# Optimization experiments

Hardware: AMD Instinct MI355X
Metric: run time of the kernel (lower is better)

## Reference

```python
import jax, jax.numpy as jnp
import numpy as np

NHEAD = 8  # heads (module default)


def _ln(x, g, b):
    m = x.mean(-1, keepdims=True)
    v = ((x - m) ** 2).mean(-1, keepdims=True)
    return (x - m) / jnp.sqrt(v + 1e-5) * g + b


def setup_inputs() -> dict:
    B, N, D, L, JE = 256, 133, 256, 6, 32
    DIN = 2 + 3 + JE  # in_proj input dim
    ks = jax.random.split(jax.random.key(0), 16)
    # chain skeleton adjacency (connected) + Floyd-Warshall hop distances
    a = np.zeros((N, N), np.float32)
    i = np.arange(N - 1)
    a[i, i + 1] = 1.0
    a[i + 1, i] = 1.0
    dist = np.full((N, N), 1e6, np.float32)
    dist[a > 0] = 1.0
    np.fill_diagonal(dist, 0.0)
    for kk in range(N):
        dist = np.minimum(dist, dist[:, kk:kk + 1] + dist[kk:kk + 1, :])
    w = lambda k, sh: jax.random.normal(k, sh, jnp.float32) * 0.02
    return dict(
        x2d=jax.random.normal(ks[0], (B, N, 2), jnp.float32),
        y3d=jax.random.normal(ks[1], (B, N, 3), jnp.float32),
        joint_emb=w(ks[2], (N, JE)),
        in_w=w(ks[3], (DIN, D)), in_b=jnp.zeros((D,), jnp.float32),
        cls_tok=w(ks[4], (1, 1, D)),
        noedge_bias=jnp.float32(-2.0), deg_scale=jnp.float32(0.2), gamma=jnp.float32(0.8),
        v2n=jnp.zeros((1,), jnp.float32), n2v=jnp.zeros((1,), jnp.float32), vself=jnp.zeros((1,), jnp.float32),
        ln1_g=jnp.ones((L, D), jnp.float32), ln1_b=jnp.zeros((L, D), jnp.float32),
        wq=w(ks[5], (L, D, D)), bq=jnp.zeros((L, D), jnp.float32),
        wk=w(ks[6], (L, D, D)), bk=jnp.zeros((L, D), jnp.float32),
        wv=w(ks[7], (L, D, D)), bv=jnp.zeros((L, D), jnp.float32),
        wo=w(ks[8], (L, D, D)), bo=jnp.zeros((L, D), jnp.float32),
        ln2_g=jnp.ones((L, D), jnp.float32), ln2_b=jnp.zeros((L, D), jnp.float32),
        mlp_w1=w(ks[9], (L, D, D)), mlp_b1=jnp.zeros((L, D), jnp.float32),  # mlp_ratio=1.0 -> hidden=D
        mlp_w2=w(ks[10], (L, D, D)), mlp_b2=jnp.zeros((L, D), jnp.float32),
        lnf_g=jnp.ones((D,), jnp.float32), lnf_b=jnp.zeros((D,), jnp.float32),
        head_w1=w(ks[11], (D, D)), head_b1=jnp.zeros((D,), jnp.float32),
        head_w2=w(ks[12], (D, 1)), head_b2=jnp.zeros((1,), jnp.float32),
        adj=jnp.asarray(a), dist=jnp.asarray(dist),
    )


def reference(x2d, y3d, joint_emb, in_w, in_b, cls_tok, noedge_bias, deg_scale, gamma,
              v2n, n2v, vself, ln1_g, ln1_b, wq, bq, wk, bk, wv, bv, wo, bo,
              ln2_g, ln2_b, mlp_w1, mlp_b1, mlp_w2, mlp_b2, lnf_g, lnf_b,
              head_w1, head_b1, head_w2, head_b2, adj, dist):
    B, N, _ = x2d.shape
    D = in_w.shape[1]
    dk = D // NHEAD
    T = N + 1
    # token features: [x2d, y3d, joint_embedding(arange(N))]
    je = jnp.broadcast_to(joint_emb[None], (B, N, joint_emb.shape[-1]))
    z = jnp.concatenate([x2d, y3d, je], axis=-1) @ in_w + in_b            # (B,N,D)
    z = jnp.concatenate([jnp.broadcast_to(cls_tok, (B, 1, D)), z], axis=1)  # (B,T,D)
    # graph attention bias (soft mask + degree + SPD + VNode 'replace'); (T,T), broadcast over B,H
    deg = adj.sum(-1)
    e = -gamma * dist                                                      # SPD term (gamma learnable)
    e = jnp.where(adj > 0, e, e + noedge_bias)                             # soft non-edge penalty
    e = e + deg_scale * (deg[:, None] + deg[None, :]) / (deg.max() + 1e-6)
    bias = jnp.zeros((T, T), jnp.float32)
    bias = bias.at[1:, 1:].set(e)
    bias = bias.at[0, 1:].set(v2n[0])
    bias = bias.at[1:, 0].set(n2v[0])
    bias = bias.at[0, 0].set(vself[0])
    bias = bias[None, None]                                                # (1,1,T,T)
    inv_sqrt_dk = jnp.float32(1.0 / np.sqrt(dk))

    def block(zc, p):
        g1, b1, qw, qb, kw, kb, vw, vb, ow, ob, g2, b2, w1, bb1, w2, bb2 = p
        x = _ln(zc, g1, b1)
        q = (x @ qw + qb).reshape(B, T, NHEAD, dk)
        k = (x @ kw + kb).reshape(B, T, NHEAD, dk)
        v = (x @ vw + vb).reshape(B, T, NHEAD, dk)
        scores = jnp.einsum('bthd,bshd->bhts', q, k) * inv_sqrt_dk + bias  # (B,H,T,T)
        attn = jax.nn.softmax(scores, axis=-1)
        out = jnp.einsum('bhts,bshd->bthd', attn, v).reshape(B, T, D)
        zc = zc + out @ ow + ob
        x = _ln(zc, g2, b2)
        zc = zc + jax.nn.gelu(x @ w1 + bb1, approximate=False) @ w2 + bb2
        return zc, None

    z, _ = jax.lax.scan(block, z, (ln1_g, ln1_b, wq, bq, wk, bk, wv, bv, wo, bo,
                                   ln2_g, ln2_b, mlp_w1, mlp_b1, mlp_w2, mlp_b2))
    z = _ln(z, lnf_g, lnf_b)
    c = z[:, 0]                                                            # CLS token
    h = jax.nn.gelu(c @ head_w1 + head_b1, approximate=False)
    return h @ head_w2 + head_b2                                           # (B,1) energy
```

## Files before the change

kernel.cpp:

```cpp
#include <hip/hip_runtime.h>
#include <stdint.h>

typedef unsigned short u16;
typedef unsigned int   u32;
typedef short bf16x8 __attribute__((ext_vector_type(8)));
typedef float f32x4  __attribute__((ext_vector_type(4)));

#define NLAYER 6
#define T_TOK  134
#define MROWS  34304
#define QKV_E  196608
#define O_E    65536
#define LSTR_E 393216
#define HEAD_E_OFF 2359296
#define SPV 168

__device__ __forceinline__ float b2f(u16 u){ u32 x=((u32)u)<<16; return __builtin_bit_cast(float,x); }
__device__ __forceinline__ u16 f2b(float f){ u32 x=__builtin_bit_cast(u32,f); return (u16)((x + 0x7fffu + ((x>>16)&1u))>>16); }
__device__ __forceinline__ void mfma16(f32x4& c, bf16x8 a, bf16x8 b){
  asm("v_mfma_f32_16x16x32_bf16 %0, %1, %2, %0" : "+v"(c) : "v"(a), "v"(b));
}
__device__ __forceinline__ float gelu_f(float x){ return 0.5f*x*(1.0f+erff(x*0.70710678118654752f)); }
__device__ __forceinline__ void gload16(const u16* g, u16* l){
  __builtin_amdgcn_global_load_lds((const __attribute__((address_space(1))) u32*)g,
                                   (__attribute__((address_space(3))) u32*)l, 16, 0, 0);
}

__global__ __launch_bounds__(256) void prep_k(
    const float* __restrict__ wq, const float* __restrict__ wk, const float* __restrict__ wv,
    const float* __restrict__ wo, const float* __restrict__ w1, const float* __restrict__ w2,
    const float* __restrict__ hw1,
    const float* __restrict__ bq, const float* __restrict__ bk, const float* __restrict__ bv,
    u16* __restrict__ wpack, float* __restrict__ bqkv)
{
  const int cid = blockIdx.x*256 + threadIdx.x;
  if (cid < 294912 + 8192) {
    const float* msrc = nullptr; int NT, c, layer = 0, isqkv = 0;
    if (cid >= 294912){ msrc = hw1; NT = 16; c = cid - 294912; }
    else {
      layer = cid / 49152; int r = cid - layer*49152;
      if      (r < 24576){ NT = 48; c = r;          isqkv = 1; }
      else if (r < 32768){ NT = 16; c = r - 24576;  msrc = wo + layer*65536; }
      else if (r < 40960){ NT = 16; c = r - 32768;  msrc = w1 + layer*65536; }
      else               { NT = 16; c = r - 40960;  msrc = w2 + layer*65536; }
    }
    const int lane = c & 63, ctkk = c >> 6;
    const int ct = ctkk % NT, kk = ctkk / NT;
    const int k = kk*32 + (lane>>4)*8;
    const int n = ct*16 + (lane&15);
    u16 ov[8];
    if (isqkv){
      const int sub = n >> 8, nn = n & 255;
      const float* s3 = (sub==0 ? wq : (sub==1 ? wk : wv)) + layer*65536;
#pragma unroll
      for(int j=0;j<8;j++) ov[j] = f2b(s3[(size_t)(k+j)*256 + nn]);
    } else {
#pragma unroll
      for(int j=0;j<8;j++) ov[j] = f2b(msrc[(size_t)(k+j)*256 + n]);
    }
    *(uint4*)(wpack + (size_t)cid*8) = *(uint4*)ov;
  } else {
    const int id = cid - 303104;
    if (id >= 0 && id < 576){
#pragma unroll
      for(int j=0;j<8;j++){
        const int p = id*8 + j; const int layer = p/768; const int w = p - layer*768;
        bqkv[p] = (w<256) ? bq[layer*256+w] : (w<512) ? bk[layer*256+w-256] : bv[layer*256+w-512];
      }
    }
  }
}

__global__ __launch_bounds__(256) void deg_k(const float* __restrict__ adj, float* __restrict__ degb)
{
  __shared__ float deg[133];
  const int tid = threadIdx.x;
  if (tid < 133){
    float s = 0.f;
    for (int j=0;j<133;j++) s += adj[tid*133+j];
    deg[tid] = s; degb[tid] = s;
  }
  __syncthreads();
  if (tid == 0){ float m=0.f; for (int i=0;i<133;i++) m = fmaxf(m, deg[i]); degb[133] = 1.0f/(m + 1e-6f); }
}

__global__ __launch_bounds__(256) void bias_k(
    const float* __restrict__ adj, const float* __restrict__ dist, const float* __restrict__ degb,
    const float* __restrict__ gamma, const float* __restrict__ noedge,
    const float* __restrict__ dscale, const float* __restrict__ v2n,
    const float* __restrict__ n2v, const float* __restrict__ vself,
    float* __restrict__ biasP)
{
  const int idx = blockIdx.x*256 + threadIdx.x;
  if (idx >= 144*144) return;
  const int t = idx/144, s = idx - t*144;
  float v;
  if (s >= 134)          v = -1e30f;
  else if (t >= 134)     v = 0.f;
  else if (t==0 && s==0) v = vself[0];
  else if (t==0)         v = v2n[0];
  else if (s==0)         v = n2v[0];
  else {
    const int i = t-1, j = s-1;
    float e = -gamma[0]*dist[i*133+j];
    if (!(adj[i*133+j] > 0.f)) e += noedge[0];
    e += dscale[0]*(degb[i]+degb[j])*degb[133];
    v = e;
  }
  biasP[idx] = v;
}

__global__ __launch_bounds__(256) void embed_k(
    const float* __restrict__ x2d, const float* __restrict__ y3d,
    const float* __restrict__ je,  const float* __restrict__ inw,
    const float* __restrict__ inb, const float* __restrict__ cls,
    float* __restrict__ z)
{
  __shared__ float f[4][37];
  const int tid = threadIdx.x, g = tid>>6, lane = tid & 63;
  const int r = blockIdx.x*4 + g;
  const int b = r/134, t = r - b*134;
  if (t > 0 && lane < 37){
    const int n = t - 1;
    float v;
    if (lane < 2)      v = x2d[(size_t)(b*133+n)*2 + lane];
    else if (lane < 5) v = y3d[(size_t)(b*133+n)*3 + (lane-2)];
    else               v = je[(size_t)n*32 + (lane-5)];
    f[g][lane] = v;
  }
  __syncthreads();
  const int d4 = lane*4;
  float4 o;
  if (t == 0){
    o = *(const float4*)(cls + d4);
  } else {
    o = *(const float4*)(inb + d4);
#pragma unroll
    for (int i=0;i<37;i++){
      const float fv = f[g][i];
      const float4 w = *(const float4*)(inw + i*256 + d4);
      o.x += fv*w.x; o.y += fv*w.y; o.z += fv*w.z; o.w += fv*w.w;
    }
  }
  *(float4*)(z + (size_t)r*256 + d4) = o;
}

__global__ __launch_bounds__(256) void ln_k(
    const float* __restrict__ z, const float* __restrict__ gw, const float* __restrict__ bw,
    u16* __restrict__ out, int rmul)
{
  const int row = blockIdx.x*8 + (threadIdx.x>>5);
  const int t5 = threadIdx.x & 31;
  const float* zr = z + (size_t)row*rmul*256 + t5*8;
  float4 v0 = *(const float4*)zr;
  float4 v1 = *(const float4*)(zr+4);
  float s = v0.x+v0.y+v0.z+v0.w + v1.x+v1.y+v1.z+v1.w;
#pragma unroll
  for (int m=1;m<32;m<<=1) s += __shfl_xor(s, m, 32);
  const float mean = s*(1.f/256.f);
  float d0=v0.x-mean,d1=v0.y-mean,d2=v0.z-mean,d3=v0.w-mean;
  float d4=v1.x-mean,d5=v1.y-mean,d6=v1.z-mean,d7=v1.w-mean;
  float q = d0*d0+d1*d1+d2*d2+d3*d3+d4*d4+d5*d5+d6*d6+d7*d7;
#pragma unroll
  for (int m=1;m<32;m<<=1) q += __shfl_xor(q, m, 32);
  const float rstd = rsqrtf(q*(1.f/256.f) + 1e-5f);
  const int c = t5*8;
  float4 g0 = *(const float4*)(gw+c), g1 = *(const float4*)(gw+c+4);
  float4 b0 = *(const float4*)(bw+c), b1 = *(const float4*)(bw+c+4);
  u32 p0 = (u32)f2b(d0*rstd*g0.x+b0.x) | ((u32)f2b(d1*rstd*g0.y+b0.y)<<16);
  u32 p1 = (u32)f2b(d2*rstd*g0.z+b0.z) | ((u32)f2b(d3*rstd*g0.w+b0.w)<<16);
  u32 p2 = (u32)f2b(d4*rstd*g1.x+b1.x) | ((u32)f2b(d5*rstd*g1.y+b1.y)<<16);
  u32 p3 = (u32)f2b(d6*rstd*g1.z+b1.z) | ((u32)f2b(d7*rstd*g1.w+b1.w)<<16);
  uint4 ov; ov.x=p0; ov.y=p1; ov.z=p2; ov.w=p3;
  *(uint4*)(out + (size_t)row*256 + c) = ov;
}

template<int EPI>
__global__ __launch_bounds__(256) void gemm_k(
    const u16* __restrict__ A, const u16* __restrict__ PB, const float* __restrict__ bias,
    u16* __restrict__ Obf, float* __restrict__ Of, float* __restrict__ Z, int NT)
{
  const int N = NT*16;
  __shared__ __align__(16) u16 lsA[4096];
  __shared__ __align__(16) u16 lsB[4096];
  const int tid = threadIdx.x, lane = tid & 63, wid = tid >> 6;
  const int m0 = blockIdx.x*128, n0 = blockIdx.y*128;
  const int wr = wid >> 1, wc = wid & 1;
  f32x4 acc[4][4];
#pragma unroll
  for (int i=0;i<4;i++)
#pragma unroll
    for (int j=0;j<4;j++){ acc[i][j][0]=0.f; acc[i][j][1]=0.f; acc[i][j][2]=0.f; acc[i][j][3]=0.f; }

  const u16* gA0 = A + (size_t)(m0 + wid*32 + (lane&15))*256 + (lane>>4)*8;
  const u16* gA1 = gA0 + 16*256;
  u16* lA0 = lsA + wid*1024;
  u16* lA1 = lA0 + 512;
  const size_t bstr = (size_t)NT*512;
  const u16* gB0 = PB + ((size_t)((n0>>4) + wid)*64 + lane)*8;
  const u16* gB1 = gB0 + 4*512;
  u16* lB0 = lsB + wid*512;
  u16* lB1 = lB0 + 4*512;

  for (int kk=0; kk<8; ++kk){
    gload16(gA0 + kk*32, lA0);
    gload16(gA1 + kk*32, lA1);
    gload16(gB0 + (size_t)kk*bstr, lB0);
    gload16(gB1 + (size_t)kk*bstr, lB1);
    __syncthreads();
    bf16x8 af[4], bfr[4];
#pragma unroll
    for (int mi=0;mi<4;mi++) af[mi]  = *(const bf16x8*)(lsA + ((wr*4+mi)*64 + lane)*8);
#pragma unroll
    for (int ni=0;ni<4;ni++) bfr[ni] = *(const bf16x8*)(lsB + ((wc*4+ni)*64 + lane)*8);
#pragma unroll
    for (int mi=0;mi<4;mi++)
#pragma unroll
      for (int ni=0;ni<4;ni++)
        mfma16(acc[mi][ni], af[mi], bfr[ni]);
    __syncthreads();
  }
  const int r0 = (lane>>4)*4, c15 = lane & 15;
#pragma unroll
  for (int mi=0;mi<4;mi++){
#pragma unroll
    for (int ni=0;ni<4;ni++){
      const int col = n0 + wc*64 + ni*16 + c15;
      const float bv = bias[col];
#pragma unroll
      for (int r=0;r<4;r++){
        const int row = m0 + wr*64 + mi*16 + r0 + r;
        float v = acc[mi][ni][r] + bv;
        if constexpr (EPI==0){ Obf[(size_t)row*N + col] = f2b(v); }
        else if constexpr (EPI==1){ Z[(size_t)row*256 + col] += v; }
        else if constexpr (EPI==2){ Obf[(size_t)row*N + col] = f2b(gelu_f(v)); }
        else { Of[(size_t)row*N + col] = gelu_f(v); }
      }
    }
  }
}

__global__ __launch_bounds__(192, 3) void attn_k(
    const u16* __restrict__ qkv, const float* __restrict__ biasP, u16* __restrict__ ao)
{
  const int blk = blockIdx.x, b = blk >> 3, h = blk & 7;
  __shared__ __align__(16) u16 Pf[3*2560];
  __shared__ __align__(16) u16 Vt[32*SPV];
  const int tid = threadIdx.x, lane = tid & 63, w = tid >> 6;
  const int g = lane >> 4, c15 = lane & 15;
  const size_t base = (size_t)b*134*768 + h*32;

  if (tid < 134){
    const uint4* vr = (const uint4*)(qkv + base + (size_t)tid*768 + 512);
    uint4 w0=vr[0], w1=vr[1], w2=vr[2], w3=vr[3];
    u32 wa[8] = {w0.x,w0.y,w0.z,w0.w,w1.x,w1.y,w1.z,w1.w};
    u32 wb[8] = {w2.x,w2.y,w2.z,w2.w,w3.x,w3.y,w3.z,w3.w};
#pragma unroll
    for (int k=0;k<8;k++){
      Vt[(2*k  )*SPV + tid] = (u16)(wa[k] & 0xffffu);
      Vt[(2*k+1)*SPV + tid] = (u16)(wa[k] >> 16);
      Vt[(16+2*k  )*SPV + tid] = (u16)(wb[k] & 0xffffu);
      Vt[(16+2*k+1)*SPV + tid] = (u16)(wb[k] >> 16);
    }
  } else if (tid < 160){
#pragma unroll
    for (int d=0; d<32; d++) Vt[d*SPV + tid] = 0;
  }
  u16* Pfw = Pf + w*2560;
  const int c_r = 2*(c15>>2) + (g&1) + 8*(2*(c15&3) + (g>>1));
  if (lane >= 32){ uint4 zz; zz.x=0u; zz.y=0u; zz.z=0u; zz.w=0u;
                   *(uint4*)(Pfw + 4*512 + c_r*8) = zz; }
  __syncthreads();

  bf16x8 kf[9];
  const int kg = g*8;
#pragma unroll
  for (int st=0; st<9; st++){
    int sr = st*16 + c15; if (sr > 133) sr = 133;
    kf[st] = *(const bf16x8*)(qkv + base + (size_t)sr*768 + 256 + kg);
  }
  const float isq = 0.17677669529663687f;

  for (int i=0;i<3;i++){
    const int qt = 3*w + i;
    int qr = qt*16 + c15; if (qr > 133) qr = 133;
    const bf16x8 qf = *(const bf16x8*)(qkv + base + (size_t)qr*768 + kg);
    f32x4 s_[9];
#pragma unroll
    for (int st=0; st<9; st++){
      s_[st][0]=0.f; s_[st][1]=0.f; s_[st][2]=0.f; s_[st][3]=0.f;
      mfma16(s_[st], qf, kf[st]);
    }
    asm volatile("s_waitcnt lgkmcnt(0)" ::: "memory");
    const int hi = c15 >> 3, j7 = c15 & 7;
#pragma unroll
    for (int r=0;r<4;r++){
      const float* br = biasP + (size_t)(qt*16 + g*4 + r)*144 + c15;
      float v[9];
#pragma unroll
      for (int st=0; st<9; st++) v[st] = s_[st][r]*isq + br[st*16];
      float mx = v[0];
#pragma unroll
      for (int st=1; st<9; st++) mx = fmaxf(mx, v[st]);
      mx = fmaxf(mx, __shfl_xor(mx,1)); mx = fmaxf(mx, __shfl_xor(mx,2));
      mx = fmaxf(mx, __shfl_xor(mx,4)); mx = fmaxf(mx, __shfl_xor(mx,8));
      float sum = 0.f;
#pragma unroll
      for (int st=0; st<9; st++){ v[st] = __expf(v[st]-mx); sum += v[st]; }
      sum += __shfl_xor(sum,1); sum += __shfl_xor(sum,2);
      sum += __shfl_xor(sum,4); sum += __shfl_xor(sum,8);
      const float ivs = 1.0f/sum;
#pragma unroll
      for (int st=0; st<9; st++){
        const int hi2 = (2*st + hi) & 3;
        const int cw  = 2*g + (hi2 & 1) + 8*(2*r + (hi2 >> 1));
        Pfw[(st>>1)*512 + cw*8 + j7] = f2b(v[st]*ivs);
      }
    }
    asm volatile("s_waitcnt lgkmcnt(0)" ::: "memory");
    __builtin_amdgcn_sched_barrier(0);
    bf16x8 a5[5];
#pragma unroll
    for (int ks=0; ks<5; ks++) a5[ks] = *(const bf16x8*)(Pfw + ks*512 + c_r*8);
#pragma unroll
    for (int nt=0; nt<2; nt++){
      f32x4 o; o[0]=0.f; o[1]=0.f; o[2]=0.f; o[3]=0.f;
#pragma unroll
      for (int ks=0; ks<5; ks++){
        const bf16x8 vb = *(const bf16x8*)(Vt + (nt*16 + c15)*SPV + ks*32 + kg);
        mfma16(o, a5[ks], vb);
      }
#pragma unroll
      for (int r=0;r<4;r++){
        const int q = qt*16 + g*4 + r;
        if (q < 134) ao[((size_t)(b*134+q))*256 + h*32 + nt*16 + c15] = f2b(o[r]);
      }
    }
  }
}

__global__ __launch_bounds__(256) void head_out_k(
    const float* __restrict__ h, const float* __restrict__ w2,
    const float* __restrict__ b2, float* __restrict__ out)
{
  const int b = blockIdx.x, d = threadIdx.x;
  float v = h[(size_t)b*256 + d] * w2[d];
#pragma unroll
  for (int m=1;m<64;m<<=1) v += __shfl_xor(v, m, 64);
  __shared__ float ps[4];
  if ((d & 63) == 0) ps[d>>6] = v;
  __syncthreads();
  if (d == 0) out[b] = ps[0]+ps[1]+ps[2]+ps[3] + b2[0];
}

extern "C" void kernel_launch(void* const* d_in, const int* in_sizes, int n_in,
                              void* d_out, int out_size, void* d_ws, size_t ws_size,
                              hipStream_t stream)
{
  (void)in_sizes; (void)n_in; (void)out_size; (void)ws_size;
  const float* x2d   =(const float*)d_in[0];
  const float* y3d   =(const float*)d_in[1];
  const float* je    =(const float*)d_in[2];
  const float* inw   =(const float*)d_in[3];
  const float* inb   =(const float*)d_in[4];
  const float* cls   =(const float*)d_in[5];
  const float* noedge=(const float*)d_in[6];
  const float* dscale=(const float*)d_in[7];
  const float* gamma =(const float*)d_in[8];
  const float* v2n   =(const float*)d_in[9];
  const float* n2v   =(const float*)d_in[10];
  const float* vself =(const float*)d_in[11];
  const float* ln1g  =(const float*)d_in[12];
  const float* ln1b  =(const float*)d_in[13];
  const float* wq    =(const float*)d_in[14];
  const float* bq    =(const float*)d_in[15];
  const float* wk    =(const float*)d_in[16];
  const float* bk    =(const float*)d_in[17];
  const float* wv    =(const float*)d_in[18];
  const float* bv    =(const float*)d_in[19];
  const float* wo    =(const float*)d_in[20];
  const float* bo    =(const float*)d_in[21];
  const float* ln2g  =(const float*)d_in[22];
  const float* ln2b  =(const float*)d_in[23];
  const float* w1    =(const float*)d_in[24];
  const float* b1    =(const float*)d_in[25];
  const float* w2    =(const float*)d_in[26];
  const float* b2    =(const float*)d_in[27];
  const float* lnfg  =(const float*)d_in[28];
  const float* lnfb  =(const float*)d_in[29];
  const float* hw1   =(const float*)d_in[30];
  const float* hb1   =(const float*)d_in[31];
  const float* hw2   =(const float*)d_in[32];
  const float* hb2   =(const float*)d_in[33];
  const float* adj   =(const float*)d_in[34];
  const float* dist  =(const float*)d_in[35];

  char* wsp = (char*)d_ws; size_t off = 0;
  auto alloc = [&](size_t bytes)->char*{ char* p = wsp + off; off = (off + bytes + 255) & ~(size_t)255; return p; };
  float* z    = (float*)alloc((size_t)MROWS*256*4);
  u16*   qkv  = (u16*)  alloc((size_t)MROWS*768*2);
  u16*   xn   = (u16*)  alloc((size_t)MROWS*256*2);
  u16*   ao   = (u16*)  alloc((size_t)MROWS*256*2);
  u16*   wpack= (u16*)  alloc((size_t)2424832*2);
  float* bqkv = (float*)alloc((size_t)6*768*4);
  float* biasP= (float*)alloc((size_t)144*144*4);
  float* degb = (float*)alloc((size_t)134*4);
  u16*   cbf  = (u16*)  alloc((size_t)256*256*2);
  float* hbuf = (float*)alloc((size_t)256*256*4);
  u16*   h1   = qkv;

  prep_k<<<1187,256,0,stream>>>(wq,wk,wv,wo,w1,w2,hw1,bq,bk,bv,wpack,bqkv);
  deg_k<<<1,256,0,stream>>>(adj, degb);
  bias_k<<<81,256,0,stream>>>(adj,dist,degb,gamma,noedge,dscale,v2n,n2v,vself,biasP);
  embed_k<<<MROWS/4,256,0,stream>>>(x2d,y3d,je,inw,inb,cls,z);

  for (int l=0; l<NLAYER; ++l){
    const u16* pq = wpack + (size_t)l*LSTR_E;
    ln_k<<<MROWS/8,256,0,stream>>>(z, ln1g + l*256, ln1b + l*256, xn, 1);
    gemm_k<0><<<dim3(MROWS/128,6),256,0,stream>>>(xn, pq, bqkv + l*768, qkv, nullptr, nullptr, 48);
    attn_k<<<2048,192,0,stream>>>(qkv, biasP, ao);
    gemm_k<1><<<dim3(MROWS/128,2),256,0,stream>>>(ao, pq + QKV_E, bo + l*256, nullptr, nullptr, z, 16);
    ln_k<<<MROWS/8,256,0,stream>>>(z, ln2g + l*256, ln2b + l*256, xn, 1);
    gemm_k<2><<<dim3(MROWS/128,2),256,0,stream>>>(xn, pq + QKV_E + O_E, b1 + l*256, h1, nullptr, nullptr, 16);
    gemm_k<1><<<dim3(MROWS/128,2),256,0,stream>>>(h1, pq + QKV_E + 2*O_E, b2 + l*256, nullptr, nullptr, z, 16);
  }

  ln_k<<<32,256,0,stream>>>(z, lnfg, lnfb, cbf, 134);
  gemm_k<3><<<dim3(2,2),256,0,stream>>>(cbf, wpack + HEAD_E_OFF, hb1, nullptr, hbuf, nullptr, 16);
  head_out_k<<<256,256,0,stream>>>(hbuf, hw2, hb2, (float*)d_out);
}
```

Measured before the change: 996.7 us.

## Fuse residual-add GEMMs with following LayerNorm and embed with first LN

```diff
diff --git a/kernel.cpp b/kernel.cpp
--- a/kernel.cpp
+++ b/kernel.cpp
@@ -114,11 +114,12 @@
     const float* __restrict__ x2d, const float* __restrict__ y3d,
     const float* __restrict__ je,  const float* __restrict__ inw,
     const float* __restrict__ inb, const float* __restrict__ cls,
-    float* __restrict__ z)
+    const float* __restrict__ lg,  const float* __restrict__ lb,
+    float* __restrict__ z, u16* __restrict__ xn)
 {
   __shared__ float f[4][37];
-  const int tid = threadIdx.x, g = tid>>6, lane = tid & 63;
-  const int r = blockIdx.x*4 + g;
+  const int tid = threadIdx.x, gq = tid>>6, lane = tid & 63;
+  const int r = blockIdx.x*4 + gq;
   const int b = r/134, t = r - b*134;
   if (t > 0 && lane < 37){
     const int n = t - 1;
@@ -126,7 +127,7 @@
     if (lane < 2)      v = x2d[(size_t)(b*133+n)*2 + lane];
     else if (lane < 5) v = y3d[(size_t)(b*133+n)*3 + (lane-2)];
     else               v = je[(size_t)n*32 + (lane-5)];
-    f[g][lane] = v;
+    f[gq][lane] = v;
   }
   __syncthreads();
   const int d4 = lane*4;
@@ -137,12 +138,26 @@
     o = *(const float4*)(inb + d4);
 #pragma unroll
     for (int i=0;i<37;i++){
-      const float fv = f[g][i];
+      const float fv = f[gq][i];
       const float4 w = *(const float4*)(inw + i*256 + d4);
       o.x += fv*w.x; o.y += fv*w.y; o.z += fv*w.z; o.w += fv*w.w;
     }
   }
   *(float4*)(z + (size_t)r*256 + d4) = o;
+  float s = o.x+o.y+o.z+o.w;
+#pragma unroll
+  for (int m=1;m<64;m<<=1) s += __shfl_xor(s, m, 64);
+  const float mean = s*(1.f/256.f);
+  const float dx=o.x-mean, dy=o.y-mean, dz=o.z-mean, dw=o.w-mean;
+  float q = dx*dx+dy*dy+dz*dz+dw*dw;
+#pragma unroll
+  for (int m=1;m<64;m<<=1) q += __shfl_xor(q, m, 64);
+  const float rstd = rsqrtf(q*(1.f/256.f) + 1e-5f);
+  const float4 gv = *(const float4*)(lg + d4), bv = *(const float4*)(lb + d4);
+  u32 p0 = (u32)f2b(dx*rstd*gv.x+bv.x) | ((u32)f2b(dy*rstd*gv.y+bv.y)<<16);
+  u32 p1 = (u32)f2b(dz*rstd*gv.z+bv.z) | ((u32)f2b(dw*rstd*gv.w+bv.w)<<16);
+  uint2 ov; ov.x = p0; ov.y = p1;
+  *(uint2*)(xn + (size_t)r*256 + d4) = ov;
 }
 
 __global__ __launch_bounds__(256) void ln_k(
@@ -235,6 +250,70 @@
         else if constexpr (EPI==1){ Z[(size_t)row*256 + col] += v; }
         else if constexpr (EPI==2){ Obf[(size_t)row*N + col] = f2b(gelu_f(v)); }
         else { Of[(size_t)row*N + col] = gelu_f(v); }
+      }
+    }
+  }
+}
+
+__global__ __launch_bounds__(256) void gemmf_k(
+    const u16* __restrict__ A, const u16* __restrict__ PB, const float* __restrict__ bias,
+    float* __restrict__ Z, const float* __restrict__ lg, const float* __restrict__ lb,
+    u16* __restrict__ xn, int doLN)
+{
+  __shared__ __align__(16) u16 lsA[2048];
+  __shared__ __align__(16) u16 lsB[8192];
+  const int tid = threadIdx.x, lane = tid & 63, w = tid >> 6;
+  const int m0 = blockIdx.x*64;
+  f32x4 acc[16];
+#pragma unroll
+  for (int ni=0;ni<16;ni++){ acc[ni][0]=0.f; acc[ni][1]=0.f; acc[ni][2]=0.f; acc[ni][3]=0.f; }
+
+  const u16* gA = A + (size_t)(m0 + w*16 + (lane&15))*256 + (lane>>4)*8;
+  u16* lA = lsA + w*512;
+  const u16* gB0 = PB + (size_t)(w*4)*512 + (size_t)lane*8;
+
+  for (int kk=0; kk<8; ++kk){
+    gload16(gA + kk*32, lA);
+#pragma unroll
+    for (int i=0;i<4;i++) gload16(gB0 + (size_t)kk*8192 + i*512, lsB + (w*4+i)*512);
+    __syncthreads();
+    const bf16x8 af = *(const bf16x8*)(lsA + w*512 + lane*8);
+#pragma unroll
+    for (int ni=0;ni<16;ni++){
+      const bf16x8 bfr = *(const bf16x8*)(lsB + ni*512 + lane*8);
+      mfma16(acc[ni], af, bfr);
+    }
+    __syncthreads();
+  }
+
+  const int g4 = lane>>4, c15 = lane & 15;
+  float bvs[16];
+#pragma unroll
+  for (int ni=0;ni<16;ni++) bvs[ni] = bias[ni*16+c15];
+#pragma unroll
+  for (int r=0;r<4;r++){
+    const int row = m0 + w*16 + g4*4 + r;
+    float* zr = Z + (size_t)row*256;
+    float zv[16]; float s = 0.f;
+#pragma unroll
+    for (int ni=0;ni<16;ni++){ zv[ni] = acc[ni][r] + bvs[ni] + zr[ni*16+c15]; s += zv[ni]; }
+#pragma unroll
+    for (int ni=0;ni<16;ni++) zr[ni*16+c15] = zv[ni];
+    if (doLN){
+      s += __shfl_xor(s,1,16); s += __shfl_xor(s,2,16);
+      s += __shfl_xor(s,4,16); s += __shfl_xor(s,8,16);
+      const float mean = s*(1.f/256.f);
+      float q = 0.f;
+#pragma unroll
+      for (int ni=0;ni<16;ni++){ const float d = zv[ni]-mean; q += d*d; }
+      q += __shfl_xor(q,1,16); q += __shfl_xor(q,2,16);
+      q += __shfl_xor(q,4,16); q += __shfl_xor(q,8,16);
+      const float rstd = rsqrtf(q*(1.f/256.f) + 1e-5f);
+      u16* xr = xn + (size_t)row*256;
+#pragma unroll
+      for (int ni=0;ni<16;ni++){
+        const int col = ni*16 + c15;
+        xr[col] = f2b((zv[ni]-mean)*rstd*lg[col] + lb[col]);
       }
     }
   }
@@ -412,17 +491,18 @@
   prep_k<<<1187,256,0,stream>>>(wq,wk,wv,wo,w1,w2,hw1,bq,bk,bv,wpack,bqkv);
   deg_k<<<1,256,0,stream>>>(adj, degb);
   bias_k<<<81,256,0,stream>>>(adj,dist,degb,gamma,noedge,dscale,v2n,n2v,vself,biasP);
-  embed_k<<<MROWS/4,256,0,stream>>>(x2d,y3d,je,inw,inb,cls,z);
+  embed_k<<<MROWS/4,256,0,stream>>>(x2d,y3d,je,inw,inb,cls,ln1g,ln1b,z,xn);
 
   for (int l=0; l<NLAYER; ++l){
     const u16* pq = wpack + (size_t)l*LSTR_E;
-    ln_k<<<MROWS/8,256,0,stream>>>(z, ln1g + l*256, ln1b + l*256, xn, 1);
     gemm_k<0><<<dim3(MROWS/128,6),256,0,stream>>>(xn, pq, bqkv + l*768, qkv, nullptr, nullptr, 48);
     attn_k<<<2048,192,0,stream>>>(qkv, biasP, ao);
-    gemm_k<1><<<dim3(MROWS/128,2),256,0,stream>>>(ao, pq + QKV_E, bo + l*256, nullptr, nullptr, z, 16);
-    ln_k<<<MROWS/8,256,0,stream>>>(z, ln2g + l*256, ln2b + l*256, xn, 1);
+    gemmf_k<<<MROWS/64,256,0,stream>>>(ao, pq + QKV_E, bo + l*256, z,
+                                       ln2g + l*256, ln2b + l*256, xn, 1);
     gemm_k<2><<<dim3(MROWS/128,2),256,0,stream>>>(xn, pq + QKV_E + O_E, b1 + l*256, h1, nullptr, nullptr, 16);
-    gemm_k<1><<<dim3(MROWS/128,2),256,0,stream>>>(h1, pq + QKV_E + 2*O_E, b2 + l*256, nullptr, nullptr, z, 16);
+    const int ln_nxt = (l < 5) ? (l+1) : 0;
+    gemmf_k<<<MROWS/64,256,0,stream>>>(h1, pq + QKV_E + 2*O_E, b2 + l*256, z,
+                                       ln1g + ln_nxt*256, ln1b + ln_nxt*256, xn, (l<5)?1:0);
   }
 
   ln_k<<<32,256,0,stream>>>(z, lnfg, lnfb, cbf, 134);
```

New measurement: 979.7 us. No clear change (-1.7%).
